# Optimization experiments

Measured on AMD Instinct MI355X. Metric: run time of the kernel, lower is better.

## Reference

```python
import jax, jax.numpy as jnp
import numpy as np

N_NODES, N_GRAPHS, PER_GRAPH, N_EDGES = 20000, 200, 100, 320000
X_DIM, E_DIM, G_DIM = 32, 16, 32
NUM_EMB, HEADS, LAYERS = 64, 2, 3
EPS_GEN, EPS_LN = 1e-7, 1e-5


def _w(k, shape, scale=0.05):
    return (jax.random.normal(k, shape) * scale).astype(jnp.float32)


def _mlp3(x, W1, b1, W2, b2, W3, b3):
    h = jax.nn.leaky_relu(x @ W1 + b1)
    h = jax.nn.leaky_relu(h @ W2 + b2)
    return h @ W3 + b3


def _seg_sum(x, idx, n):
    return jax.ops.segment_sum(x, idx, num_segments=n)


def _seg_mean(x, idx, n):
    s = _seg_sum(x, idx, n)
    cnt = _seg_sum(jnp.ones((x.shape[0],), x.dtype), idx, n)
    return s / jnp.clip(cnt, 1.0, None)[:, None]


def _seg_softmax(logits, idx, n):
    # PyG softmax: subtract per-segment max, normalize with +1e-16
    m = jax.ops.segment_max(logits, idx, num_segments=n)
    m = jnp.where(jnp.isfinite(m), m, 0.0)
    e = jnp.exp(logits - m[idx])
    s = jax.ops.segment_sum(e, idx, num_segments=n)
    return e / (s[idx] + 1e-16)


def _graph_layernorm(x, batch, n_graphs):
    # PyG LayerNorm(mode='graph', affine=False): mean/var over all node-feature
    # entries of each graph.
    f = x.shape[-1]
    cnt = _seg_sum(jnp.ones((x.shape[0],), x.dtype), batch, n_graphs)
    norm = jnp.clip(cnt, 1.0, None) * f
    mean = _seg_sum(x.sum(-1), batch, n_graphs) / norm
    xc = x - mean[batch][:, None]
    var = _seg_sum((xc * xc).sum(-1), batch, n_graphs) / norm
    return xc / jnp.sqrt(var + EPS_LN)[batch][:, None]


def _forward(x, edge_attr, cond, edge_index, batch,
             x2h_W1, x2h_b1, x2h_W2, x2h_b2, x2h_W3, x2h_b3,
             e2h_W1, e2h_b1, e2h_W2, e2h_b2, e2h_W3, e2h_b3,
             c2h_W1, c2h_b1, c2h_W2, c2h_b2, c2h_W3, c2h_b3,
             gen_W, tr_Wq, tr_bq, tr_Wk, tr_bk, tr_Wv, tr_bv, tr_We, tr_Ws, tr_bs,
             lin_W, lin_b, ff_W1, ff_b1, ff_W2, ff_b2):
    N = x.shape[0]
    G = cond.shape[0]
    Naug = N + G
    o = _mlp3(x, x2h_W1, x2h_b1, x2h_W2, x2h_b2, x2h_W3, x2h_b3)
    e = _mlp3(edge_attr, e2h_W1, e2h_b1, e2h_W2, e2h_b2, e2h_W3, e2h_b3)
    c = _mlp3(cond, c2h_W1, c2h_b1, c2h_W2, c2h_b2, c2h_W3, c2h_b3)
    # virtual-node edges: node<->virtual node of its graph (virtual ids = N..N+G-1)
    u = jnp.arange(N, dtype=edge_index.dtype)
    v = batch.astype(edge_index.dtype) + N
    aug_ei = jnp.concatenate([edge_index, jnp.stack([u, v]), jnp.stack([v, u])], axis=1)
    e_p = jnp.zeros((2 * N, NUM_EMB), o.dtype).at[:, 0].set(1.0)
    aug_e = jnp.concatenate([e, e_p], axis=0)
    # add_self_loops(fill_value='mean'): self-loop attr = mean of incoming edge attrs
    loop_attr = _seg_mean(aug_e, aug_ei[1], Naug)
    loops = jnp.arange(Naug, dtype=edge_index.dtype)
    aug_ei = jnp.concatenate([aug_ei, jnp.stack([loops, loops])], axis=1)
    aug_e = jnp.concatenate([aug_e, loop_attr], axis=0)
    aug_batch = jnp.concatenate([batch, jnp.arange(G, dtype=batch.dtype)])
    o = jnp.concatenate([o, c], axis=0)  # [Naug, emb]
    src, dst = aug_ei[0], aug_ei[1]
    scale = 1.0 / float(np.sqrt(NUM_EMB))
    for i in range(LAYERS):
        # GENConv(aggr='add', norm=None, num_layers=1): sum(relu(x_j+e)+eps) + x, then Linear
        msg = jax.nn.relu(o[src] + aug_e) + EPS_GEN
        agg = (_seg_sum(msg, dst, Naug) + o) @ gen_W[i]
        # TransformerConv(2*emb -> emb, heads, edge_dim=emb, concat=True)
        xin = jnp.concatenate([o, agg], axis=1)  # [Naug, 2*emb]
        q = (xin @ tr_Wq[i] + tr_bq[i]).reshape(Naug, HEADS, NUM_EMB)
        k = (xin @ tr_Wk[i] + tr_bk[i]).reshape(Naug, HEADS, NUM_EMB)
        vv = (xin @ tr_Wv[i] + tr_bv[i]).reshape(Naug, HEADS, NUM_EMB)
        eh = (aug_e @ tr_We[i]).reshape(-1, HEADS, NUM_EMB)  # [E, H, C]
        kj = k[src] + eh
        alpha = _seg_softmax(jnp.einsum('ehc,ehc->eh', q[dst], kj) * scale, dst, Naug)
        tout = _seg_sum((vv[src] + eh) * alpha[..., None], dst, Naug)
        tout = tout.reshape(Naug, HEADS * NUM_EMB) + xin @ tr_Ws[i] + tr_bs[i]
        # residual + graph LayerNorm, then FFN + graph LayerNorm
        o = _graph_layernorm(o + tout @ lin_W[i] + lin_b[i], aug_batch, G)
        ff = jax.nn.leaky_relu(o @ ff_W1[i] + ff_b1[i]) @ ff_W2[i] + ff_b2[i]
        o = _graph_layernorm(o + ff, aug_batch, G)
    node_o, virt = o[:N], o[N:]
    glob = jnp.concatenate([_seg_mean(node_o, batch, G), virt, c], axis=1)
    o_final = jnp.concatenate([node_o, c[batch]], axis=1)
    return (o_final, glob)


def setup_inputs() -> dict:
    key = jax.random.key(0)
    ks = iter(jax.random.split(key, 64))
    inp = {}
    inp['x'] = jax.random.normal(next(ks), (N_NODES, X_DIM), dtype=jnp.float32)
    inp['edge_attr'] = jax.random.normal(next(ks), (N_EDGES, E_DIM), dtype=jnp.float32)
    inp['cond'] = jax.random.normal(next(ks), (N_GRAPHS, G_DIM), dtype=jnp.float32)
    src = jax.random.randint(next(ks), (N_EDGES,), 0, N_NODES)
    dst = (src // PER_GRAPH) * PER_GRAPH + jax.random.randint(next(ks), (N_EDGES,), 0, PER_GRAPH)
    inp['edge_index'] = jnp.stack([src, dst]).astype(jnp.int32)
    inp['batch'] = jnp.repeat(jnp.arange(N_GRAPHS, dtype=jnp.int32), PER_GRAPH)
    for p, nin in [('x2h', X_DIM), ('e2h', E_DIM), ('c2h', G_DIM)]:
        inp[p + '_W1'] = _w(next(ks), (nin, NUM_EMB)); inp[p + '_b1'] = _w(next(ks), (NUM_EMB,))
        inp[p + '_W2'] = _w(next(ks), (NUM_EMB, NUM_EMB)); inp[p + '_b2'] = _w(next(ks), (NUM_EMB,))
        inp[p + '_W3'] = _w(next(ks), (NUM_EMB, NUM_EMB)); inp[p + '_b3'] = _w(next(ks), (NUM_EMB,))
    HC = HEADS * NUM_EMB
    inp['gen_W'] = _w(next(ks), (LAYERS, NUM_EMB, NUM_EMB))
    inp['tr_Wq'] = _w(next(ks), (LAYERS, 2 * NUM_EMB, HC)); inp['tr_bq'] = _w(next(ks), (LAYERS, HC))
    inp['tr_Wk'] = _w(next(ks), (LAYERS, 2 * NUM_EMB, HC)); inp['tr_bk'] = _w(next(ks), (LAYERS, HC))
    inp['tr_Wv'] = _w(next(ks), (LAYERS, 2 * NUM_EMB, HC)); inp['tr_bv'] = _w(next(ks), (LAYERS, HC))
    inp['tr_We'] = _w(next(ks), (LAYERS, NUM_EMB, HC))
    inp['tr_Ws'] = _w(next(ks), (LAYERS, 2 * NUM_EMB, HC)); inp['tr_bs'] = _w(next(ks), (LAYERS, HC))
    inp['lin_W'] = _w(next(ks), (LAYERS, HC, NUM_EMB)); inp['lin_b'] = _w(next(ks), (LAYERS, NUM_EMB))
    inp['ff_W1'] = _w(next(ks), (LAYERS, NUM_EMB, 4 * NUM_EMB)); inp['ff_b1'] = _w(next(ks), (LAYERS, 4 * NUM_EMB))
    inp['ff_W2'] = _w(next(ks), (LAYERS, 4 * NUM_EMB, NUM_EMB)); inp['ff_b2'] = _w(next(ks), (LAYERS, NUM_EMB))
    return inp


def reference(x, edge_attr, cond, edge_index, batch,
              x2h_W1, x2h_b1, x2h_W2, x2h_b2, x2h_W3, x2h_b3,
              e2h_W1, e2h_b1, e2h_W2, e2h_b2, e2h_W3, e2h_b3,
              c2h_W1, c2h_b1, c2h_W2, c2h_b2, c2h_W3, c2h_b3,
              gen_W, tr_Wq, tr_bq, tr_Wk, tr_bk, tr_Wv, tr_bv, tr_We, tr_Ws, tr_bs,
              lin_W, lin_b, ff_W1, ff_b1, ff_W2, ff_b2):
    return _forward(x, edge_attr, cond, edge_index, batch,
                    x2h_W1, x2h_b1, x2h_W2, x2h_b2, x2h_W3, x2h_b3,
                    e2h_W1, e2h_b1, e2h_W2, e2h_b2, e2h_W3, e2h_b3,
                    c2h_W1, c2h_b1, c2h_W2, c2h_b2, c2h_W3, c2h_b3,
                    gen_W, tr_Wq, tr_bq, tr_Wk, tr_bk, tr_Wv, tr_bv, tr_We, tr_Ws, tr_bs,
                    lin_W, lin_b, ff_W1, ff_b1, ff_W2, ff_b2)
```

## Files before the change

### kernel.cpp

```cpp
#include <hip/hip_runtime.h>
#include <cstddef>

#define NN   20000
#define NG   200
#define NE   320000
#define NAUG 20200
#define NE2  360000
#define EAUG 380200
#define DD   64
#define HC   128
#define QS   640

typedef float  f32x4 __attribute__((ext_vector_type(4)));
typedef short  s16x8 __attribute__((ext_vector_type(8)));

static __device__ __forceinline__ unsigned short bf16r(float f){
  unsigned u = __float_as_uint(f);
  u += 0x7FFFu + ((u >> 16) & 1u);
  return (unsigned short)(u >> 16);
}
static __device__ __forceinline__ float4 b2f4(ushort4 u){
  return make_float4(__uint_as_float((unsigned)u.x << 16),
                     __uint_as_float((unsigned)u.y << 16),
                     __uint_as_float((unsigned)u.z << 16),
                     __uint_as_float((unsigned)u.w << 16));
}
static __device__ __forceinline__ ushort4 f2b4(float4 v){
  ushort4 s; s.x=bf16r(v.x); s.y=bf16r(v.y); s.z=bf16r(v.z); s.w=bf16r(v.w); return s;
}
static __device__ __forceinline__ float d4(float4 a, float4 b){
  return a.x*b.x + a.y*b.y + a.z*b.z + a.w*b.w;
}
static __device__ __forceinline__ float4 f4a(float4 a, float4 b, float t){
  return make_float4(a.x + b.x*t, a.y + b.y*t, a.z + b.z*t, a.w + b.w*t);
}
static __device__ __forceinline__ float4 f4s(float4 a, float s){
  return make_float4(a.x*s, a.y*s, a.z*s, a.w*s);
}

#define WTAB_INIT { \
  {0,0,128,128,136,128,0},{0,0,128,128,136,128,16384},{0,0,128,128,136,128,32768}, \
  {1,0,128,128,136,128,0},{1,0,128,128,136,128,16384},{1,0,128,128,136,128,32768}, \
  {2,0,128,128,136,128,0},{2,0,128,128,136,128,16384},{2,0,128,128,136,128,32768}, \
  {3,0,128,128,136,128,0},{3,0,128,128,136,128,16384},{3,0,128,128,136,128,32768}, \
  {4,0,64,64,72,64,0},{4,0,64,64,72,64,4096},{4,0,64,64,72,64,8192}, \
  {5,0,128,64,136,64,0},{5,0,128,64,136,64,8192},{5,0,128,64,136,64,16384}, \
  {6,0,64,256,72,256,0},{6,0,64,256,72,256,16384},{6,0,64,256,72,256,32768}, \
  {7,0,256,64,264,64,0},{7,0,256,64,264,64,16384},{7,0,256,64,264,64,32768}, \
  {8,0,64,64,72,128,0},{8,0,64,64,72,128,64},{8,0,64,64,72,128,8192},{8,0,64,64,72,128,8256},{8,0,64,64,72,128,16384},{8,0,64,64,72,128,16448}, \
  {9,0,32,64,40,64,0},{10,0,64,64,72,64,0},{11,0,64,64,72,64,0}, \
  {12,0,16,64,40,64,0},{13,0,64,64,72,64,0},{14,0,64,64,72,64,0}, \
  {15,0,32,64,40,64,0},{16,0,64,64,72,64,0},{17,0,64,64,72,64,0} }

static const int WTAB_H[39][7] = WTAB_INIT;
__device__ static const int WTAB_D[39][7] = WTAB_INIT;

struct WPtrs { const float* p[18]; };

__global__ void wconv_all_k(WPtrs wp, unsigned short* __restrict__ outbase){
  int b = blockIdx.x;
  int acc = 0; unsigned ooff = 0;
  #pragma unroll 1
  for (int j = 0; j < 39; j++){
    int e  = WTAB_D[j][3] * WTAB_D[j][4];
    int nb = (e + 255) >> 8;
    if (b < acc + nb){
      int idx = (b - acc)*256 + threadIdx.x;
      if (idx < e){
        int KP = WTAB_D[j][4];
        int n = idx / KP, k = idx % KP;
        float v = 0.f;
        if (k < WTAB_D[j][2]){
          const float* s = wp.p[WTAB_D[j][0]];
          int st = WTAB_D[j][5], so = WTAB_D[j][6];
          v = (WTAB_D[j][1] == 0) ? s[(size_t)so + (size_t)k*st + n]
                                  : s[(size_t)so + (size_t)n*st + k];
        }
        outbase[ooff + idx] = bf16r(v);
      }
      return;
    }
    acc += nb; ooff += (unsigned)e;
  }
}

__global__ void qecomb_k(const float* __restrict__ trWq, const float* __restrict__ trbq,
                         const float* __restrict__ trWe,
                         unsigned short* __restrict__ qweb, float* __restrict__ bqeb){
  int L = blockIdx.y;
  int n = blockIdx.x;
  int i = threadIdx.x;
  int h = n >> 6, d = n & 63;
  const float* Wq = trWq + (size_t)L*128*128;
  const float* We = trWe + (size_t)L*64*128;
  float acc = 0.f;
  for (int c = 0; c < 64; c++)
    acc += Wq[(size_t)i*128 + h*64 + c] * We[(size_t)d*128 + h*64 + c];
  qweb[(size_t)L*128*136 + n*136 + i] = bf16r(acc);
  if (i < 8) qweb[(size_t)L*128*136 + n*136 + 128 + i] = 0;
  if (i == 0){
    const float* bq = trbq + (size_t)L*128;
    float b = 0.f;
    for (int c = 0; c < 64; c++) b += bq[h*64 + c] * We[(size_t)d*128 + h*64 + c];
    bqeb[L*128 + n] = b;
  }
}

template<int NT>
__launch_bounds__(256)
__global__ void gemm_mfma_k(const float* __restrict__ A, const float* __restrict__ A2,
                            int M, int K, int lda,
                            const unsigned short* __restrict__ WtG,
                            const float* __restrict__ bias, int act,
                            const float* __restrict__ res, const float* __restrict__ res2,
                            int rstride, float* __restrict__ out, int ostride){
  extern __shared__ unsigned short smem[];
  const int KC  = (K > 128) ? 128 : K;
  const int KPc = KC + 8;
  const int KP  = K + 8;
  unsigned short* Wts  = smem;
  unsigned short* Asub = smem + NT*KPc;
  const int tid = threadIdx.x;
  const int wid = tid >> 6, lane = tid & 63;
  const int lrow = lane & 15, quad = lane >> 4;
  const int m0 = blockIdx.x * 64;
  f32x4 acc[NT/16];
  #pragma unroll
  for (int t = 0; t < NT/16; t++) acc[t] = (f32x4){0.f,0.f,0.f,0.f};

  for (int k0 = 0; k0 < K; k0 += KC){
    const int wv = NT*KPc/8, wrow = KPc/8;
    for (int i = tid; i < wv; i += 256){
      int n = i / wrow, c8 = i % wrow;
      *(uint4*)&Wts[n*KPc + c8*8] = *(const uint4*)&WtG[(size_t)n*KP + k0 + c8*8];
    }
    const int av = 64*KC/4, arow = KC/4;
    for (int i = tid; i < av; i += 256){
      int r = i / arow, c4i = i % arow;
      int m = m0 + r, k = k0 + c4i*4;
      float4 v = make_float4(0.f,0.f,0.f,0.f);
      if (m < M){
        v = *(const float4*)(A + (size_t)m*lda + k);
        if (A2){ float4 w = *(const float4*)(A2 + (size_t)m*lda + k);
                 v.x += w.x; v.y += w.y; v.z += w.z; v.w += w.w; }
      }
      *(ushort4*)&Asub[r*KPc + c4i*4] = f2b4(v);
    }
    __syncthreads();
    const int ksteps = KC >> 5;
    for (int ks = 0; ks < ksteps; ks++){
      s16x8 a = *(const s16x8*)&Asub[(wid*16 + lrow)*KPc + ks*32 + quad*8];
      #pragma unroll
      for (int nt = 0; nt < NT/16; nt++){
        s16x8 b = *(const s16x8*)&Wts[(nt*16 + lrow)*KPc + ks*32 + quad*8];
        acc[nt] = __builtin_amdgcn_mfma_f32_16x16x32_bf16(a, b, acc[nt], 0, 0, 0);
      }
    }
    __syncthreads();
  }

  const int mb = m0 + wid*16 + quad*4;
  #pragma unroll
  for (int nt = 0; nt < NT/16; nt++){
    int n = nt*16 + lrow;
    #pragma unroll
    for (int r = 0; r < 4; r++){
      int m = mb + r;
      if (m < M){
        float v = acc[nt][r];
        if (bias) v += bias[n];
        if (act)  v = v > 0.f ? v : 0.01f*v;
        if (res)  v += res [(size_t)m*rstride + n];
        if (res2) v += res2[(size_t)m*rstride + n];
        out[(size_t)m*ostride + n] = v;
      }
    }
  }
}

struct PW5 { const unsigned short* w[5]; const float* b[5]; };

__launch_bounds__(256)
__global__ void qkvs5_k(const float* __restrict__ A, int M, PW5 pw,
                        float* __restrict__ out){
  __shared__ __align__(16) unsigned short Wts[128*136];
  __shared__ __align__(16) unsigned short Asub[64*136];
  const unsigned short* WtG = pw.w[blockIdx.y];
  const float* bias = pw.b[blockIdx.y];
  const int tid = threadIdx.x;
  const int wid = tid >> 6, lane = tid & 63;
  const int lrow = lane & 15, quad = lane >> 4;
  const int m0 = blockIdx.x * 64;
  for (int i = tid; i < 128*17; i += 256){
    int n = i/17, c8 = i%17;
    *(uint4*)&Wts[n*136 + c8*8] = *(const uint4*)&WtG[(size_t)n*136 + c8*8];
  }
  for (int i = tid; i < 64*32; i += 256){
    int r = i >> 5, c4 = (i & 31)*4;
    int m = m0 + r;
    float4 v = make_float4(0.f,0.f,0.f,0.f);
    if (m < M) v = *(const float4*)(A + (size_t)m*128 + c4);
    *(ushort4*)&Asub[r*136 + c4] = f2b4(v);
  }
  __syncthreads();
  f32x4 acc[8];
  #pragma unroll
  for (int t=0;t<8;t++) acc[t] = (f32x4){0.f,0.f,0.f,0.f};
  #pragma unroll
  for (int ks = 0; ks < 4; ks++){
    s16x8 a = *(const s16x8*)&Asub[(wid*16 + lrow)*136 + ks*32 + quad*8];
    #pragma unroll
    for (int nt = 0; nt < 8; nt++){
      s16x8 b = *(const s16x8*)&Wts[(nt*16 + lrow)*136 + ks*32 + quad*8];
      acc[nt] = __builtin_amdgcn_mfma_f32_16x16x32_bf16(a, b, acc[nt], 0, 0, 0);
    }
  }
  const int mb = m0 + wid*16 + quad*4;
  const int yoff = blockIdx.y*128;
  #pragma unroll
  for (int nt = 0; nt < 8; nt++){
    int n = nt*16 + lrow;
    #pragma unroll
    for (int r = 0; r < 4; r++){
      int m = mb + r;
      if (m < M) out[(size_t)m*QS + yoff + n] = acc[nt][r] + bias[n];
    }
  }
}

struct PW2 { const unsigned short* w[2]; };

__launch_bounds__(256)
__global__ void tout2_k(const float* __restrict__ wv, int M, PW2 pw,
                        const float* __restrict__ t1, const float* __restrict__ qkvs,
                        float* __restrict__ tout){
  __shared__ __align__(16) unsigned short Wts[64*72];
  __shared__ __align__(16) unsigned short Asub[64*72];
  const unsigned short* WtG = pw.w[blockIdx.y];
  const int tid = threadIdx.x;
  const int wid = tid >> 6, lane = tid & 63;
  const int lrow = lane & 15, quad = lane >> 4;
  const int m0 = blockIdx.x * 64;
  const int yoff = blockIdx.y * 64;
  for (int i = tid; i < 64*9; i += 256){
    int n = i/9, c8 = i%9;
    *(uint4*)&Wts[n*72 + c8*8] = *(const uint4*)&WtG[(size_t)n*72 + c8*8];
  }
  for (int i = tid; i < 64*16; i += 256){
    int r = i >> 4, c4 = (i & 15)*4;
    int m = m0 + r;
    float4 v = make_float4(0.f,0.f,0.f,0.f);
    if (m < M) v = *(const float4*)(wv + (size_t)m*HC + yoff + c4);
    *(ushort4*)&Asub[r*72 + c4] = f2b4(v);
  }
  __syncthreads();
  f32x4 acc[4];
  #pragma unroll
  for (int t=0;t<4;t++) acc[t] = (f32x4){0.f,0.f,0.f,0.f};
  #pragma unroll
  for (int ks = 0; ks < 2; ks++){
    s16x8 a = *(const s16x8*)&Asub[(wid*16 + lrow)*72 + ks*32 + quad*8];
    #pragma unroll
    for (int nt = 0; nt < 4; nt++){
      s16x8 b = *(const s16x8*)&Wts[(nt*16 + lrow)*72 + ks*32 + quad*8];
      acc[nt] = __builtin_amdgcn_mfma_f32_16x16x32_bf16(a, b, acc[nt], 0, 0, 0);
    }
  }
  const int mb = m0 + wid*16 + quad*4;
  #pragma unroll
  for (int nt = 0; nt < 4; nt++){
    int n = nt*16 + lrow;
    #pragma unroll
    for (int r = 0; r < 4; r++){
      int m = mb + r;
      if (m < M)
        tout[(size_t)m*HC + yoff + n] = acc[nt][r]
          + t1[(size_t)m*HC + yoff + n] + qkvs[(size_t)m*QS + 384 + yoff + n];
    }
  }
}

__launch_bounds__(256)
__global__ void mlp3_mfma_k(const float* __restrict__ X, int M, int Din,
                            const unsigned short* __restrict__ w1t,
                            const unsigned short* __restrict__ w2t,
                            const unsigned short* __restrict__ w3t,
                            const float* __restrict__ b1, const float* __restrict__ b2,
                            const float* __restrict__ b3,
                            const int* __restrict__ perm, float* __restrict__ out,
                            unsigned short* __restrict__ outb){
  __shared__ __align__(16) unsigned short W1s[64*40], W2s[64*72], W3s[64*72];
  __shared__ __align__(16) unsigned short xs[64*40], hs[64*72];
  __shared__ float bsh[192];
  const int tid = threadIdx.x;
  for (int i = tid; i < 320; i += 256)  *(uint4*)&W1s[i*8] = *(const uint4*)&w1t[i*8];
  for (int i = tid; i < 576; i += 256){ *(uint4*)&W2s[i*8] = *(const uint4*)&w2t[i*8];
                                        *(uint4*)&W3s[i*8] = *(const uint4*)&w3t[i*8]; }
  if (tid < 64){ bsh[tid] = b1[tid]; bsh[64+tid] = b2[tid]; bsh[128+tid] = b3[tid]; }
  const int m0 = blockIdx.x * 64;
  for (int i = tid; i < 512; i += 256){
    int r = i >> 3, c4 = (i & 7) * 4;
    int m = m0 + r;
    float4 v = make_float4(0.f,0.f,0.f,0.f);
    if (m < M && c4 < Din) v = *(const float4*)(X + (size_t)m*Din + c4);
    *(ushort4*)&xs[r*40 + c4] = f2b4(v);
  }
  __syncthreads();
  const int wid = tid >> 6, lane = tid & 63;
  const int lrow = lane & 15, quad = lane >> 4;
  f32x4 acc[4];

  #pragma unroll
  for (int t = 0; t < 4; t++) acc[t] = (f32x4){0.f,0.f,0.f,0.f};
  {
    s16x8 a = *(const s16x8*)&xs[(wid*16 + lrow)*40 + quad*8];
    #pragma unroll
    for (int nt = 0; nt < 4; nt++){
      s16x8 b = *(const s16x8*)&W1s[(nt*16 + lrow)*40 + quad*8];
      acc[nt] = __builtin_amdgcn_mfma_f32_16x16x32_bf16(a, b, acc[nt], 0, 0, 0);
    }
  }
  #pragma unroll
  for (int nt = 0; nt < 4; nt++){
    int n = nt*16 + lrow;
    #pragma unroll
    for (int r = 0; r < 4; r++){
      float v = acc[nt][r] + bsh[n];
      v = v > 0.f ? v : 0.01f*v;
      hs[(wid*16 + quad*4 + r)*72 + n] = bf16r(v);
    }
  }
  __syncthreads();

  #pragma unroll
  for (int t = 0; t < 4; t++) acc[t] = (f32x4){0.f,0.f,0.f,0.f};
  #pragma unroll
  for (int ks = 0; ks < 2; ks++){
    s16x8 a = *(const s16x8*)&hs[(wid*16 + lrow)*72 + ks*32 + quad*8];
    #pragma unroll
    for (int nt = 0; nt < 4; nt++){
      s16x8 b = *(const s16x8*)&W2s[(nt*16 + lrow)*72 + ks*32 + quad*8];
      acc[nt] = __builtin_amdgcn_mfma_f32_16x16x32_bf16(a, b, acc[nt], 0, 0, 0);
    }
  }
  __syncthreads();
  #pragma unroll
  for (int nt = 0; nt < 4; nt++){
    int n = nt*16 + lrow;
    #pragma unroll
    for (int r = 0; r < 4; r++){
      float v = acc[nt][r] + bsh[64 + n];
      v = v > 0.f ? v : 0.01f*v;
      hs[(wid*16 + quad*4 + r)*72 + n] = bf16r(v);
    }
  }
  __syncthreads();

  #pragma unroll
  for (int t = 0; t < 4; t++) acc[t] = (f32x4){0.f,0.f,0.f,0.f};
  #pragma unroll
  for (int ks = 0; ks < 2; ks++){
    s16x8 a = *(const s16x8*)&hs[(wid*16 + lrow)*72 + ks*32 + quad*8];
    #pragma unroll
    for (int nt = 0; nt < 4; nt++){
      s16x8 b = *(const s16x8*)&W3s[(nt*16 + lrow)*72 + ks*32 + quad*8];
      acc[nt] = __builtin_amdgcn_mfma_f32_16x16x32_bf16(a, b, acc[nt], 0, 0, 0);
    }
  }
  #pragma unroll
  for (int nt = 0; nt < 4; nt++){
    int n = nt*16 + lrow;
    #pragma unroll
    for (int r = 0; r < 4; r++){
      int m = m0 + wid*16 + quad*4 + r;
      if (m < M){
        int orow = perm ? perm[m] : m;
        float v = acc[nt][r] + bsh[128 + n];
        if (outb) outb[(size_t)orow*64 + n] = bf16r(v);
        else      out [(size_t)orow*64 + n] = v;
      }
    }
  }
}

__global__ void build_edges_k(const int* __restrict__ ei, const int* __restrict__ batch,
                              int* __restrict__ srcA, int* __restrict__ dstA){
  int idx = blockIdx.x*256 + threadIdx.x;
  if (idx >= EAUG) return;
  int s, d;
  if (idx < NE)          { s = ei[idx];              d = ei[NE+idx]; }
  else if (idx < NE+NN)  { int i = idx-NE;           s = i;            d = batch[i]+NN; }
  else if (idx < NE2)    { int i = idx-(NE+NN);      s = batch[i]+NN;  d = i; }
  else                   { int i = idx-NE2;          s = i;            d = i; }
  srcA[idx]=s; dstA[idx]=d;
}

__global__ void count_k(const int* __restrict__ dstA, int* __restrict__ cnt){
  int e = blockIdx.x*256 + threadIdx.x;
  if (e < EAUG) atomicAdd(&cnt[dstA[e]], 1);
}

__global__ void scan_k(const int* __restrict__ cnt, int* __restrict__ rowptr){
  __shared__ int part[1024];
  int tid = threadIdx.x;
  const int per = (NAUG + 1023) / 1024;
  int base = tid * per;
  int s = 0;
  for (int i=0;i<per;i++){ int idx=base+i; if (idx<NAUG) s += cnt[idx]; }
  part[tid] = s;
  __syncthreads();
  for (int off=1; off<1024; off<<=1){
    int v = (tid>=off) ? part[tid-off] : 0;
    __syncthreads();
    part[tid] += v;
    __syncthreads();
  }
  int run = (tid==0) ? 0 : part[tid-1];
  for (int i=0;i<per;i++){
    int idx=base+i;
    if (idx<NAUG){ rowptr[idx]=run; run += cnt[idx]; }
  }
  if (tid==0) rowptr[NAUG] = EAUG;
}

__global__ void scatter_k(const int* __restrict__ srcA, const int* __restrict__ dstA,
                          const int* __restrict__ rowptr, int* __restrict__ cursor,
                          int* __restrict__ esrc, int* __restrict__ epos,
                          int* __restrict__ pdst){
  int e = blockIdx.x*256 + threadIdx.x;
  if (e >= EAUG) return;
  int d = dstA[e];
  int pos = rowptr[d] + atomicAdd(&cursor[d], 1);
  esrc[pos] = srcA[e];
  pdst[pos] = d;
  epos[e]   = pos;
}

__global__ void set_ep_k(const int* __restrict__ epos, unsigned short* __restrict__ aug_b){
  int idx = blockIdx.x*256 + threadIdx.x;
  if (idx >= 2*NN*DD) return;
  int i = idx >> 6, c = idx & 63;
  aug_b[(size_t)epos[NE + i]*DD + c] = (c==0) ? (unsigned short)0x3F80 : (unsigned short)0;
}

__launch_bounds__(256)
__global__ void loopmean_k(const int* __restrict__ rowptr, const int* __restrict__ epos,
                           unsigned short* __restrict__ aug_b){
  int tid = threadIdx.x;
  int d = blockIdx.x*16 + (tid>>4);
  if (d >= NAUG) return;
  int t4 = (tid & 15)*4;
  int beg = rowptr[d], end = rowptr[d+1];
  int sp = epos[NE2 + d];
  float4 s = make_float4(0.f,0.f,0.f,0.f);
  for (int p=beg; p<end; p++){
    float4 a = b2f4(*(const ushort4*)(aug_b + (size_t)p*DD + t4));
    float w = (p == sp) ? 0.f : 1.f;
    s.x += w*a.x; s.y += w*a.y; s.z += w*a.z; s.w += w*a.w;
  }
  int n = end - beg - 1;
  float cv = (n < 1) ? 1.f : (float)n;
  *(ushort4*)(aug_b + (size_t)sp*DD + t4) = f2b4(f4s(s, 1.f/cv));
}

__launch_bounds__(512)
__global__ void msg_graph_k(const float* __restrict__ o, const unsigned short* __restrict__ aug_b,
                            const int* __restrict__ rowptr,
                            const int* __restrict__ esrc, float* __restrict__ aggsum){
  __shared__ __align__(16) float OS[101*72];
  __shared__ unsigned char EL[3072];
  const int g = blockIdx.x >> 1, half = blockIdx.x & 1;
  const int tid = threadIdx.x;
  for (int i = tid; i < 101*16; i += 512){
    int ln = i >> 4, c4 = (i & 15)*4;
    int row = (ln < 100) ? g*100 + ln : NN + g;
    *(float4*)&OS[ln*72 + c4] = *(const float4*)(o + (size_t)row*DD + c4);
  }
  const int baseA = rowptr[g*100];
  const int lenA  = rowptr[g*100 + 100] - baseA;
  const int baseB = rowptr[NN + g];
  const int lenB  = rowptr[NN + g + 1] - baseB;
  const bool useL = (lenA + lenB) <= 3072;
  if (useL){
    for (int i = tid; i < lenA; i += 512){
      int s = esrc[baseA + i];
      EL[i] = (unsigned char)((s >= NN) ? 100 : (s - g*100));
    }
    for (int i = tid; i < lenB; i += 512){
      int s = esrc[baseB + i];
      EL[lenA + i] = (unsigned char)((s >= NN) ? 100 : (s - g*100));
    }
  }
  __syncthreads();
  const int gr = tid >> 4, t4 = (tid & 15)*4;
  const int ld0 = half ? 51 : 0, ld1 = half ? 101 : 51;
  for (int ld = ld0 + gr; ld < ld1; ld += 32){
    int d, pbeg, pend, eofs;
    if (ld < 100){ d = g*100 + ld; pbeg = rowptr[d]; pend = rowptr[d+1]; eofs = -baseA; }
    else         { d = NN + g;     pbeg = baseB;     pend = baseB + lenB; eofs = lenA - baseB; }
    float4 acc = make_float4(0.f,0.f,0.f,0.f);
    for (int p = pbeg; p < pend; p++){
      int ls;
      if (useL) ls = EL[p + eofs];
      else { int s = esrc[p]; ls = (s >= NN) ? 100 : (s - g*100); }
      float4 ov = *(const float4*)&OS[ls*72 + t4];
      float4 ae = b2f4(*(const ushort4*)(aug_b + (size_t)p*DD + t4));
      acc.x += fmaxf(ov.x+ae.x, 0.f) + 1e-7f;
      acc.y += fmaxf(ov.y+ae.y, 0.f) + 1e-7f;
      acc.z += fmaxf(ov.z+ae.z, 0.f) + 1e-7f;
      acc.w += fmaxf(ov.w+ae.w, 0.f) + 1e-7f;
    }
    *(float4*)(aggsum + (size_t)d*DD + t4) = acc;
  }
}

__global__ void copy_o_xin_k(const float* __restrict__ o, float* __restrict__ xin){
  int idx = blockIdx.x*256 + threadIdx.x;
  if (idx >= NAUG*DD) return;
  int n = idx >> 6, c = idx & 63;
  xin[(size_t)n*HC + c] = o[idx];
}

__launch_bounds__(512)
__global__ void scoredot_k(const float* __restrict__ qkvs,
                           const unsigned short* __restrict__ aug_b,
                           const int* __restrict__ pdst, const int* __restrict__ esrc,
                           float2* __restrict__ lg){
  int p = blockIdx.x*32 + (threadIdx.x >> 4);
  if (p >= EAUG) return;
  int t4 = (threadIdx.x & 15)*4;
  int d = pdst[p], s = esrc[p];
  const float* qr = qkvs + (size_t)d*QS;
  const float* kr = qkvs + (size_t)s*QS + 128;
  float4 q0  = *(const float4*)(qr + t4);
  float4 q1  = *(const float4*)(qr + 64 + t4);
  float4 qe0 = *(const float4*)(qr + 512 + t4);
  float4 qe1 = *(const float4*)(qr + 576 + t4);
  float4 k0  = *(const float4*)(kr + t4);
  float4 k1  = *(const float4*)(kr + 64 + t4);
  float4 ae  = b2f4(*(const ushort4*)(aug_b + (size_t)p*DD + t4));
  float p0 = d4(q0,k0) + d4(qe0,ae);
  float p1 = d4(q1,k1) + d4(qe1,ae);
  p0 += __shfl_xor(p0,8); p0 += __shfl_xor(p0,4); p0 += __shfl_xor(p0,2); p0 += __shfl_xor(p0,1);
  p1 += __shfl_xor(p1,8); p1 += __shfl_xor(p1,4); p1 += __shfl_xor(p1,2); p1 += __shfl_xor(p1,1);
  if ((threadIdx.x & 15) == 0) lg[p] = make_float2(p0*0.125f, p1*0.125f);
}

__launch_bounds__(512)
__global__ void attn_lite_k(const float* __restrict__ qkvs, const float2* __restrict__ lg,
                            const int* __restrict__ rowptr, const int* __restrict__ esrc,
                            float* __restrict__ t1, float2* __restrict__ m2,
                            float2* __restrict__ linv2){
  __shared__ __align__(16) unsigned short VS[101*128];
  __shared__ unsigned char EL[3072];
  const int g = blockIdx.x >> 1, half = blockIdx.x & 1;
  const int tid = threadIdx.x;
  for (int i = tid; i < 101*32; i += 512){
    int ln = i >> 5, c4 = (i & 31)*4;
    int row = (ln < 100) ? g*100 + ln : NN + g;
    float4 v = *(const float4*)(qkvs + (size_t)row*QS + 256 + c4);
    *(ushort4*)&VS[ln*128 + c4] = f2b4(v);
  }
  const int baseA = rowptr[g*100];
  const int lenA  = rowptr[g*100 + 100] - baseA;
  const int baseB = rowptr[NN + g];
  const int lenB  = rowptr[NN + g + 1] - baseB;
  const bool useL = (lenA + lenB) <= 3072;
  if (useL){
    for (int i = tid; i < lenA; i += 512){
      int s = esrc[baseA + i];
      EL[i] = (unsigned char)((s >= NN) ? 100 : (s - g*100));
    }
    for (int i = tid; i < lenB; i += 512){
      int s = esrc[baseB + i];
      EL[lenA + i] = (unsigned char)((s >= NN) ? 100 : (s - g*100));
    }
  }
  __syncthreads();
  const int gr = tid >> 4, t4 = (tid & 15)*4;
  const int ld0 = half ? 51 : 0, ld1 = half ? 101 : 51;
  for (int ld = ld0 + gr; ld < ld1; ld += 32){
    int d, pbeg, pend, eofs;
    if (ld < 100){ d = g*100 + ld; pbeg = rowptr[d]; pend = rowptr[d+1]; eofs = -baseA; }
    else         { d = NN + g;     pbeg = baseB;     pend = baseB + lenB; eofs = lenA - baseB; }
    float m0 = -1e30f, m1 = -1e30f;
    for (int p = pbeg; p < pend; p++){
      float2 lv = lg[p];
      m0 = fmaxf(m0, lv.x); m1 = fmaxf(m1, lv.y);
    }
    float l0 = 0.f, l1 = 0.f;
    float4 a0 = make_float4(0.f,0.f,0.f,0.f), a1 = a0;
    for (int p = pbeg; p < pend; p++){
      float2 lv = lg[p];
      int ls;
      if (useL) ls = EL[p + eofs];
      else { int s = esrc[p]; ls = (s >= NN) ? 100 : (s - g*100); }
      const unsigned short* vr = &VS[ls*128];
      float4 v0 = b2f4(*(const ushort4*)(vr + t4));
      float4 v1 = b2f4(*(const ushort4*)(vr + 64 + t4));
      float e0 = __expf(lv.x - m0);
      float e1 = __expf(lv.y - m1);
      l0 += e0; a0 = f4a(a0, v0, e0);
      l1 += e1; a1 = f4a(a1, v1, e1);
    }
    float i0 = 1.f/(l0 + 1e-16f), i1 = 1.f/(l1 + 1e-16f);
    *(float4*)(t1 + (size_t)d*HC + t4)      = f4s(a0, i0);
    *(float4*)(t1 + (size_t)d*HC + 64 + t4) = f4s(a1, i1);
    if ((tid & 15) == 0){
      m2[d]    = make_float2(m0, m1);
      linv2[d] = make_float2(i0, i1);
    }
  }
}

__launch_bounds__(256)
__global__ void wsum_k(const unsigned short* __restrict__ aug_b, const float2* __restrict__ lg,
                       const float2* __restrict__ m2, const float2* __restrict__ linv2,
                       const int* __restrict__ rowptr, float* __restrict__ wbuf){
  int tid = threadIdx.x;
  int d = blockIdx.x*16 + (tid>>4);
  if (d >= NAUG) return;
  int t4 = (tid & 15)*4;
  float2 m = m2[d];
  float2 li = linv2[d];
  float4 w0 = make_float4(0.f,0.f,0.f,0.f), w1 = w0;
  int beg = rowptr[d], end = rowptr[d+1];
  for (int p = beg; p < end; p++){
    float2 lv = lg[p];
    float4 ae = b2f4(*(const ushort4*)(aug_b + (size_t)p*DD + t4));
    float a0 = __expf(lv.x - m.x) * li.x;
    float a1 = __expf(lv.y - m.y) * li.y;
    w0 = f4a(w0, ae, a0);
    w1 = f4a(w1, ae, a1);
  }
  *(float4*)(wbuf + (size_t)d*HC + t4)      = w0;
  *(float4*)(wbuf + (size_t)d*HC + 64 + t4) = w1;
}

__global__ void ln_k(const float* __restrict__ y, float* __restrict__ o,
                     float* __restrict__ xin){
  int g = blockIdx.x, tid = threadIdx.x;
  float sum=0.f, ss=0.f;
  for (int i=tid; i<101*64; i+=256){
    int nd=i>>6, c=i&63;
    int row = (nd<100) ? g*100+nd : NN+g;
    float v = y[(size_t)row*DD + c];
    sum += v; ss += v*v;
  }
  #pragma unroll
  for (int off=32; off; off>>=1){ sum += __shfl_xor(sum, off); ss += __shfl_xor(ss, off); }
  __shared__ float s1[4], s2[4];
  if ((tid&63)==0){ s1[tid>>6]=sum; s2[tid>>6]=ss; }
  __syncthreads();
  sum = s1[0]+s1[1]+s1[2]+s1[3];
  ss  = s2[0]+s2[1]+s2[2]+s2[3];
  const float inv = 1.f/6464.f;
  float mean = sum*inv;
  float var  = ss*inv - mean*mean;
  float rstd = rsqrtf(var + 1e-5f);
  for (int i=tid; i<101*64; i+=256){
    int nd=i>>6, c=i&63;
    int row = (nd<100) ? g*100+nd : NN+g;
    float v = (y[(size_t)row*DD + c] - mean)*rstd;
    o[(size_t)row*DD + c] = v;
    if (xin) xin[(size_t)row*HC + c] = v;
  }
}

__global__ void copy_c_o_k(const float* __restrict__ c_emb, float* __restrict__ o){
  int idx = blockIdx.x*256 + threadIdx.x;
  if (idx >= NG*DD) return;
  o[(size_t)NN*DD + idx] = c_emb[idx];
}

__global__ void glob_k(const float* __restrict__ o, const float* __restrict__ c_emb,
                       float* __restrict__ gout){
  int g = blockIdx.x, c = threadIdx.x;
  float acc = 0.f;
  for (int t=0;t<100;t++) acc += o[(size_t)(g*100+t)*DD + c];
  gout[(size_t)g*192 + c]       = acc / 100.f;
  gout[(size_t)g*192 + 64 + c]  = o[(size_t)(NN+g)*DD + c];
  gout[(size_t)g*192 + 128 + c] = c_emb[(size_t)g*DD + c];
}
__global__ void ofinal_k(const float* __restrict__ o, const float* __restrict__ c_emb,
                         const int* __restrict__ batch, float* __restrict__ out){
  int idx = blockIdx.x*256 + threadIdx.x;
  if (idx >= NN*HC) return;
  int n = idx>>7, j = idx&127;
  out[idx] = (j<64) ? o[(size_t)n*DD + j] : c_emb[(size_t)batch[n]*DD + (j-64)];
}

static inline int cdiv(int a, int b){ return (a+b-1)/b; }

static inline void gemm_mfma(int N, const float* A, const float* A2, int M, int K, int lda,
                             const unsigned short* Wt, const float* bias, int act,
                             const float* res, const float* res2, int rstride,
                             float* out, int ostride, hipStream_t st){
  int KC = (K > 128) ? 128 : K;
  int KPc = KC + 8;
  size_t sh = (size_t)(N*KPc + 64*KPc) * 2;
  int grid = cdiv(M, 64);
  if (N == 64)
    gemm_mfma_k<64><<<grid,256,sh,st>>>(A,A2,M,K,lda,Wt,bias,act,res,res2,rstride,out,ostride);
  else if (N == 128)
    gemm_mfma_k<128><<<grid,256,sh,st>>>(A,A2,M,K,lda,Wt,bias,act,res,res2,rstride,out,ostride);
  else
    gemm_mfma_k<256><<<grid,256,sh,st>>>(A,A2,M,K,lda,Wt,bias,act,res,res2,rstride,out,ostride);
}

extern "C" void kernel_launch(void* const* d_in, const int* in_sizes, int n_in,
                              void* d_out, int out_size, void* d_ws, size_t ws_size,
                              hipStream_t stream){
  (void)in_sizes; (void)n_in; (void)out_size;
  const float* x         = (const float*)d_in[0];
  const float* edge_attr = (const float*)d_in[1];
  const float* cond      = (const float*)d_in[2];
  const int*   edge_index= (const int*)  d_in[3];
  const int*   batch     = (const int*)  d_in[4];
  const float* xW1=(const float*)d_in[5],  *xb1=(const float*)d_in[6],
             * xW2=(const float*)d_in[7],  *xb2=(const float*)d_in[8],
             * xW3=(const float*)d_in[9],  *xb3=(const float*)d_in[10];
  const float* eW1=(const float*)d_in[11], *eb1=(const float*)d_in[12],
             * eW2=(const float*)d_in[13], *eb2=(const float*)d_in[14],
             * eW3=(const float*)d_in[15], *eb3=(const float*)d_in[16];
  const float* cW1=(const float*)d_in[17], *cb1=(const float*)d_in[18],
             * cW2=(const float*)d_in[19], *cb2=(const float*)d_in[20],
             * cW3=(const float*)d_in[21], *cb3=(const float*)d_in[22];
  const float* gen_W=(const float*)d_in[23];
  const float* trWq=(const float*)d_in[24], *trbq=(const float*)d_in[25];
  const float* trWk=(const float*)d_in[26], *trbk=(const float*)d_in[27];
  const float* trWv=(const float*)d_in[28], *trbv=(const float*)d_in[29];
  const float* trWe=(const float*)d_in[30];
  const float* trWs=(const float*)d_in[31], *trbs=(const float*)d_in[32];
  const float* linW=(const float*)d_in[33], *linb=(const float*)d_in[34];
  const float* ffW1=(const float*)d_in[35], *ffb1=(const float*)d_in[36];
  const float* ffW2=(const float*)d_in[37], *ffb2=(const float*)d_in[38];
  float* out = (float*)d_out;

  float* ws = (float*)d_ws;
  size_t off = 0;
  auto alloc = [&](size_t n)->float*{ float* p = ws + off; off += (n + 63) & ~(size_t)63; return p; };
  int*      srcA  = (int*)alloc(EAUG);
  int*      dstA  = (int*)alloc(EAUG);
  int*      cnt   = (int*)alloc(NAUG);
  int*      rowptr= (int*)alloc(NAUG+1);
  int*      cursor= (int*)alloc(NAUG);
  int*      esrc  = (int*)alloc(EAUG);
  int*      epos  = (int*)alloc(EAUG);
  int*      pdst  = (int*)alloc(EAUG);
  unsigned short* aug_b = (unsigned short*)alloc((size_t)EAUG*DD/2);
  float*    o     = alloc((size_t)NAUG*DD);
  float*    c_emb = alloc((size_t)NG*DD);
  float*    ybuf  = alloc((size_t)NAUG*DD);
  float*    aggsum= alloc((size_t)NAUG*DD);
  float*    xin   = alloc((size_t)NAUG*HC);
  float*    xqkvs = alloc((size_t)NAUG*QS);
  float*    toutb = alloc((size_t)NAUG*HC);
  float*    t1    = alloc((size_t)NAUG*HC);
  float*    wbuf  = alloc((size_t)NAUG*HC);
  float*    ffh   = alloc((size_t)NAUG*256);
  float2*   lgb   = (float2*)alloc((size_t)EAUG*2);
  float2*   m2v   = (float2*)alloc((size_t)NAUG*2);
  float2*   li2v  = (float2*)alloc((size_t)NAUG*2);
  unsigned short* warena = (unsigned short*)alloc(210432);
  unsigned short* qweb   = (unsigned short*)alloc(3*128*136/2 + 64);
  float*    bqeb  = alloc(3*128);
  if (off*sizeof(float) > ws_size) return;

  const unsigned short* wptr[39];
  int wblk = 0;
  { size_t woff = 0;
    for (int j = 0; j < 39; j++){
      wptr[j] = warena + woff;
      int e = WTAB_H[j][3]*WTAB_H[j][4];
      woff += (size_t)e;
      wblk += cdiv(e, 256);
    } }

  WPtrs wp;
  wp.p[0]=trWq; wp.p[1]=trWk; wp.p[2]=trWv; wp.p[3]=trWs; wp.p[4]=gen_W;
  wp.p[5]=linW; wp.p[6]=ffW1; wp.p[7]=ffW2; wp.p[8]=trWe;
  wp.p[9]=xW1; wp.p[10]=xW2; wp.p[11]=xW3;
  wp.p[12]=eW1; wp.p[13]=eW2; wp.p[14]=eW3;
  wp.p[15]=cW1; wp.p[16]=cW2; wp.p[17]=cW3;
  wconv_all_k<<<wblk,256,0,stream>>>(wp, warena);
  qecomb_k<<<dim3(128,3),128,0,stream>>>(trWq, trbq, trWe, qweb, bqeb);

  build_edges_k<<<cdiv(EAUG,256),256,0,stream>>>(edge_index, batch, srcA, dstA);
  hipMemsetAsync(cnt, 0, sizeof(int)*NAUG, stream);
  hipMemsetAsync(cursor, 0, sizeof(int)*NAUG, stream);
  count_k<<<cdiv(EAUG,256),256,0,stream>>>(dstA, cnt);
  scan_k<<<1,1024,0,stream>>>(cnt, rowptr);
  scatter_k<<<cdiv(EAUG,256),256,0,stream>>>(srcA, dstA, rowptr, cursor, esrc, epos, pdst);

  mlp3_mfma_k<<<cdiv(NN,64),256,0,stream>>>(x,        NN, 32, wptr[30],wptr[31],wptr[32], xb1,xb2,xb3, nullptr, o,     nullptr);
  mlp3_mfma_k<<<cdiv(NG,64),256,0,stream>>>(cond,     NG, 32, wptr[36],wptr[37],wptr[38], cb1,cb2,cb3, nullptr, c_emb, nullptr);
  mlp3_mfma_k<<<cdiv(NE,64),256,0,stream>>>(edge_attr,NE, 16, wptr[33],wptr[34],wptr[35], eb1,eb2,eb3, epos,    nullptr, aug_b);
  set_ep_k<<<cdiv(2*NN*DD,256),256,0,stream>>>(epos, aug_b);
  loopmean_k<<<cdiv(NAUG,16),256,0,stream>>>(rowptr, epos, aug_b);
  copy_c_o_k<<<cdiv(NG*DD,256),256,0,stream>>>(c_emb, o);
  copy_o_xin_k<<<cdiv(NAUG*DD,256),256,0,stream>>>(o, xin);

  for (int L=0; L<3; L++){
    const float* lb_i = linb + (size_t)L*DD;
    const float* f1b  = ffb1 + (size_t)L*256;
    const float* f2b  = ffb2 + (size_t)L*DD;
    const unsigned short* genT = wptr[12+L], *linT = wptr[15+L], *ff1T = wptr[18+L], *ff2T = wptr[21+L];
    PW5 pw5;
    pw5.w[0]=wptr[0+L]; pw5.w[1]=wptr[3+L]; pw5.w[2]=wptr[6+L]; pw5.w[3]=wptr[9+L];
    pw5.w[4]=qweb + (size_t)L*128*136;
    pw5.b[0]=trbq+(size_t)L*HC; pw5.b[1]=trbk+(size_t)L*HC;
    pw5.b[2]=trbv+(size_t)L*HC; pw5.b[3]=trbs+(size_t)L*HC;
    pw5.b[4]=bqeb + (size_t)L*128;
    PW2 pwT; pwT.w[0]=wptr[24+2*L]; pwT.w[1]=wptr[25+2*L];

    msg_graph_k<<<2*NG,512,0,stream>>>(o, aug_b, rowptr, esrc, aggsum);
    gemm_mfma( 64, aggsum, o, NAUG, 64, 64, genT, nullptr, 0, nullptr, nullptr, 0, xin+64, HC, stream);
    qkvs5_k<<<dim3(cdiv(NAUG,64),5),256,0,stream>>>(xin, NAUG, pw5, xqkvs);
    scoredot_k<<<cdiv(EAUG,32),512,0,stream>>>(xqkvs, aug_b, pdst, esrc, lgb);
    attn_lite_k<<<2*NG,512,0,stream>>>(xqkvs, lgb, rowptr, esrc, t1, m2v, li2v);
    wsum_k<<<cdiv(NAUG,16),256,0,stream>>>(aug_b, lgb, m2v, li2v, rowptr, wbuf);
    tout2_k<<<dim3(cdiv(NAUG,64),2),256,0,stream>>>(wbuf, NAUG, pwT, t1, xqkvs, toutb);
    gemm_mfma( 64, toutb, nullptr, NAUG, 128, 128, linT, lb_i, 0, o, nullptr, DD, ybuf, DD, stream);
    ln_k<<<NG,256,0,stream>>>(ybuf, o, nullptr);
    gemm_mfma(256, o,   nullptr, NAUG,  64,  64, ff1T, f1b, 1, nullptr, nullptr, 0, ffh, 256, stream);
    gemm_mfma( 64, ffh, nullptr, NAUG, 256, 256, ff2T, f2b, 0, o, nullptr, DD, ybuf, DD, stream);
    ln_k<<<NG,256,0,stream>>>(ybuf, o, xin);
  }

  glob_k<<<NG,64,0,stream>>>(o, c_emb, out + (size_t)NN*HC);
  ofinal_k<<<cdiv(NN*HC,256),256,0,stream>>>(o, c_emb, batch, out);
}
```

Before: 1.316 ms.

## Fuse edge-weighted sum into attention kernel and restructure CSR build

New measurement: 1.283 ms. 1.03x faster.

```diff
diff --git a/kernel.cpp b/kernel.cpp
--- a/kernel.cpp
+++ b/kernel.cpp
@@ -290,30 +290,36 @@
                             const int* __restrict__ perm, float* __restrict__ out,
                             unsigned short* __restrict__ outb){
   __shared__ __align__(16) unsigned short W1s[64*40], W2s[64*72], W3s[64*72];
-  __shared__ __align__(16) unsigned short xs[64*40], hs[64*72];
+  __shared__ __align__(16) unsigned short xs[4][16*40];
+  __shared__ __align__(16) unsigned short hs[4][16*72];
   __shared__ float bsh[192];
   const int tid = threadIdx.x;
+  const int wid = tid >> 6, lane = tid & 63;
+  const int lrow = lane & 15, quad = lane >> 4;
   for (int i = tid; i < 320; i += 256)  *(uint4*)&W1s[i*8] = *(const uint4*)&w1t[i*8];
   for (int i = tid; i < 576; i += 256){ *(uint4*)&W2s[i*8] = *(const uint4*)&w2t[i*8];
                                         *(uint4*)&W3s[i*8] = *(const uint4*)&w3t[i*8]; }
   if (tid < 64){ bsh[tid] = b1[tid]; bsh[64+tid] = b2[tid]; bsh[128+tid] = b3[tid]; }
-  const int m0 = blockIdx.x * 64;
-  for (int i = tid; i < 512; i += 256){
-    int r = i >> 3, c4 = (i & 7) * 4;
+
+  const int m0 = blockIdx.x*64 + wid*16;
+  {
+    int r = lane >> 2, c8 = (lane & 3) * 8;
     int m = m0 + r;
-    float4 v = make_float4(0.f,0.f,0.f,0.f);
-    if (m < M && c4 < Din) v = *(const float4*)(X + (size_t)m*Din + c4);
-    *(ushort4*)&xs[r*40 + c4] = f2b4(v);
+    float4 va = make_float4(0.f,0.f,0.f,0.f), vb = va;
+    if (m < M && c8 < Din){
+      va = *(const float4*)(X + (size_t)m*Din + c8);
+      vb = *(const float4*)(X + (size_t)m*Din + c8 + 4);
+    }
+    *(ushort4*)&xs[wid][r*40 + c8]     = f2b4(va);
+    *(ushort4*)&xs[wid][r*40 + c8 + 4] = f2b4(vb);
   }
   __syncthreads();
-  const int wid = tid >> 6, lane = tid & 63;
-  const int lrow = lane & 15, quad = lane >> 4;
+
   f32x4 acc[4];
-
   #pragma unroll
   for (int t = 0; t < 4; t++) acc[t] = (f32x4){0.f,0.f,0.f,0.f};
   {
-    s16x8 a = *(const s16x8*)&xs[(wid*16 + lrow)*40 + quad*8];
+    s16x8 a = *(const s16x8*)&xs[wid][lrow*40 + quad*8];
     #pragma unroll
     for (int nt = 0; nt < 4; nt++){
       s16x8 b = *(const s16x8*)&W1s[(nt*16 + lrow)*40 + quad*8];
@@ -327,23 +333,20 @@
     for (int r = 0; r < 4; r++){
       float v = acc[nt][r] + bsh[n];
       v = v > 0.f ? v : 0.01f*v;
-      hs[(wid*16 + quad*4 + r)*72 + n] = bf16r(v);
-    }
-  }
-  __syncthreads();
-
+      hs[wid][(quad*4 + r)*72 + n] = bf16r(v);
+    }
+  }
   #pragma unroll
   for (int t = 0; t < 4; t++) acc[t] = (f32x4){0.f,0.f,0.f,0.f};
   #pragma unroll
   for (int ks = 0; ks < 2; ks++){
-    s16x8 a = *(const s16x8*)&hs[(wid*16 + lrow)*72 + ks*32 + quad*8];
+    s16x8 a = *(const s16x8*)&hs[wid][lrow*72 + ks*32 + quad*8];
     #pragma unroll
     for (int nt = 0; nt < 4; nt++){
       s16x8 b = *(const s16x8*)&W2s[(nt*16 + lrow)*72 + ks*32 + quad*8];
       acc[nt] = __builtin_amdgcn_mfma_f32_16x16x32_bf16(a, b, acc[nt], 0, 0, 0);
     }
   }
-  __syncthreads();
   #pragma unroll
   for (int nt = 0; nt < 4; nt++){
     int n = nt*16 + lrow;
@@ -351,16 +354,14 @@
     for (int r = 0; r < 4; r++){
       float v = acc[nt][r] + bsh[64 + n];
       v = v > 0.f ? v : 0.01f*v;
-      hs[(wid*16 + quad*4 + r)*72 + n] = bf16r(v);
-    }
-  }
-  __syncthreads();
-
+      hs[wid][(quad*4 + r)*72 + n] = bf16r(v);
+    }
+  }
   #pragma unroll
   for (int t = 0; t < 4; t++) acc[t] = (f32x4){0.f,0.f,0.f,0.f};
   #pragma unroll
   for (int ks = 0; ks < 2; ks++){
-    s16x8 a = *(const s16x8*)&hs[(wid*16 + lrow)*72 + ks*32 + quad*8];
+    s16x8 a = *(const s16x8*)&hs[wid][lrow*72 + ks*32 + quad*8];
     #pragma unroll
     for (int nt = 0; nt < 4; nt++){
       s16x8 b = *(const s16x8*)&W3s[(nt*16 + lrow)*72 + ks*32 + quad*8];
@@ -372,7 +373,7 @@
     int n = nt*16 + lrow;
     #pragma unroll
     for (int r = 0; r < 4; r++){
-      int m = m0 + wid*16 + quad*4 + r;
+      int m = m0 + quad*4 + r;
       if (m < M){
         int orow = perm ? perm[m] : m;
         float v = acc[nt][r] + bsh[128 + n];
@@ -384,7 +385,8 @@
 }
 
 __global__ void build_edges_k(const int* __restrict__ ei, const int* __restrict__ batch,
-                              int* __restrict__ srcA, int* __restrict__ dstA){
+                              int* __restrict__ srcA, int* __restrict__ dstA,
+                              int* __restrict__ cnt){
   int idx = blockIdx.x*256 + threadIdx.x;
   if (idx >= EAUG) return;
   int s, d;
@@ -393,11 +395,7 @@
   else if (idx < NE2)    { int i = idx-(NE+NN);      s = batch[i]+NN;  d = i; }
   else                   { int i = idx-NE2;          s = i;            d = i; }
   srcA[idx]=s; dstA[idx]=d;
-}
-
-__global__ void count_k(const int* __restrict__ dstA, int* __restrict__ cnt){
-  int e = blockIdx.x*256 + threadIdx.x;
-  if (e < EAUG) atomicAdd(&cnt[dstA[e]], 1);
+  atomicAdd(&cnt[d], 1);
 }
 
 __global__ void scan_k(const int* __restrict__ cnt, int* __restrict__ rowptr){
@@ -423,17 +421,30 @@
   if (tid==0) rowptr[NAUG] = EAUG;
 }
 
-__global__ void scatter_k(const int* __restrict__ srcA, const int* __restrict__ dstA,
+__global__ void scatter_k(const int* __restrict__ dstA,
                           const int* __restrict__ rowptr, int* __restrict__ cursor,
-                          int* __restrict__ esrc, int* __restrict__ epos,
-                          int* __restrict__ pdst){
+                          int* __restrict__ eid, int* __restrict__ epos){
   int e = blockIdx.x*256 + threadIdx.x;
   if (e >= EAUG) return;
   int d = dstA[e];
   int pos = rowptr[d] + atomicAdd(&cursor[d], 1);
-  esrc[pos] = srcA[e];
-  pdst[pos] = d;
-  epos[e]   = pos;
+  eid[pos] = e;
+  epos[e]  = pos;
+}
+
+__global__ void fill_esrc_k(const int* __restrict__ eid, const int* __restrict__ srcA,
+                            int* __restrict__ esrc){
+  int p = blockIdx.x*256 + threadIdx.x;
+  if (p < EAUG) esrc[p] = srcA[eid[p]];
+}
+
+__launch_bounds__(256)
+__global__ void fill_pdst_k(const int* __restrict__ rowptr, int* __restrict__ pdst){
+  int d = blockIdx.x*16 + (threadIdx.x >> 4);
+  if (d >= NAUG) return;
+  int lane = threadIdx.x & 15;
+  int beg = rowptr[d], end = rowptr[d+1];
+  for (int p = beg + lane; p < end; p += 16) pdst[p] = d;
 }
 
 __global__ void set_ep_k(const int* __restrict__ epos, unsigned short* __restrict__ aug_b){
@@ -548,9 +559,9 @@
 
 __launch_bounds__(512)
 __global__ void attn_lite_k(const float* __restrict__ qkvs, const float2* __restrict__ lg,
+                            const unsigned short* __restrict__ aug_b,
                             const int* __restrict__ rowptr, const int* __restrict__ esrc,
-                            float* __restrict__ t1, float2* __restrict__ m2,
-                            float2* __restrict__ linv2){
+                            float* __restrict__ t1, float* __restrict__ wbuf){
   __shared__ __align__(16) unsigned short VS[101*128];
   __shared__ unsigned char EL[3072];
   const int g = blockIdx.x >> 1, half = blockIdx.x & 1;
@@ -589,7 +600,7 @@
       m0 = fmaxf(m0, lv.x); m1 = fmaxf(m1, lv.y);
     }
     float l0 = 0.f, l1 = 0.f;
-    float4 a0 = make_float4(0.f,0.f,0.f,0.f), a1 = a0;
+    float4 a0 = make_float4(0.f,0.f,0.f,0.f), a1 = a0, w0 = a0, w1 = a0;
     for (int p = pbeg; p < pend; p++){
       float2 lv = lg[p];
       int ls;
@@ -598,43 +609,18 @@
       const unsigned short* vr = &VS[ls*128];
       float4 v0 = b2f4(*(const ushort4*)(vr + t4));
       float4 v1 = b2f4(*(const ushort4*)(vr + 64 + t4));
+      float4 ae = b2f4(*(const ushort4*)(aug_b + (size_t)p*DD + t4));
       float e0 = __expf(lv.x - m0);
       float e1 = __expf(lv.y - m1);
-      l0 += e0; a0 = f4a(a0, v0, e0);
-      l1 += e1; a1 = f4a(a1, v1, e1);
+      l0 += e0; a0 = f4a(a0, v0, e0); w0 = f4a(w0, ae, e0);
+      l1 += e1; a1 = f4a(a1, v1, e1); w1 = f4a(w1, ae, e1);
     }
     float i0 = 1.f/(l0 + 1e-16f), i1 = 1.f/(l1 + 1e-16f);
-    *(float4*)(t1 + (size_t)d*HC + t4)      = f4s(a0, i0);
-    *(float4*)(t1 + (size_t)d*HC + 64 + t4) = f4s(a1, i1);
-    if ((tid & 15) == 0){
-      m2[d]    = make_float2(m0, m1);
-      linv2[d] = make_float2(i0, i1);
-    }
-  }
-}
-
-__launch_bounds__(256)
-__global__ void wsum_k(const unsigned short* __restrict__ aug_b, const float2* __restrict__ lg,
-                       const float2* __restrict__ m2, const float2* __restrict__ linv2,
-                       const int* __restrict__ rowptr, float* __restrict__ wbuf){
-  int tid = threadIdx.x;
-  int d = blockIdx.x*16 + (tid>>4);
-  if (d >= NAUG) return;
-  int t4 = (tid & 15)*4;
-  float2 m = m2[d];
-  float2 li = linv2[d];
-  float4 w0 = make_float4(0.f,0.f,0.f,0.f), w1 = w0;
-  int beg = rowptr[d], end = rowptr[d+1];
-  for (int p = beg; p < end; p++){
-    float2 lv = lg[p];
-    float4 ae = b2f4(*(const ushort4*)(aug_b + (size_t)p*DD + t4));
-    float a0 = __expf(lv.x - m.x) * li.x;
-    float a1 = __expf(lv.y - m.y) * li.y;
-    w0 = f4a(w0, ae, a0);
-    w1 = f4a(w1, ae, a1);
-  }
-  *(float4*)(wbuf + (size_t)d*HC + t4)      = w0;
-  *(float4*)(wbuf + (size_t)d*HC + 64 + t4) = w1;
+    *(float4*)(t1   + (size_t)d*HC + t4)      = f4s(a0, i0);
+    *(float4*)(t1   + (size_t)d*HC + 64 + t4) = f4s(a1, i1);
+    *(float4*)(wbuf + (size_t)d*HC + t4)      = f4s(w0, i0);
+    *(float4*)(wbuf + (size_t)d*HC + 64 + t4) = f4s(w1, i1);
+  }
 }
 
 __global__ void ln_k(const float* __restrict__ y, float* __restrict__ o,
@@ -745,6 +731,7 @@
   int*      cnt   = (int*)alloc(NAUG);
   int*      rowptr= (int*)alloc(NAUG+1);
   int*      cursor= (int*)alloc(NAUG);
+  int*      eid   = (int*)alloc(EAUG);
   int*      esrc  = (int*)alloc(EAUG);
   int*      epos  = (int*)alloc(EAUG);
   int*      pdst  = (int*)alloc(EAUG);
@@ -760,8 +747,6 @@
   float*    wbuf  = alloc((size_t)NAUG*HC);
   float*    ffh   = alloc((size_t)NAUG*256);
   float2*   lgb   = (float2*)alloc((size_t)EAUG*2);
-  float2*   m2v   = (float2*)alloc((size_t)NAUG*2);
-  float2*   li2v  = (float2*)alloc((size_t)NAUG*2);
   unsigned short* warena = (unsigned short*)alloc(210432);
   unsigned short* qweb   = (unsigned short*)alloc(3*128*136/2 + 64);
   float*    bqeb  = alloc(3*128);
@@ -786,12 +771,13 @@
   wconv_all_k<<<wblk,256,0,stream>>>(wp, warena);
   qecomb_k<<<dim3(128,3),128,0,stream>>>(trWq, trbq, trWe, qweb, bqeb);
 
-  build_edges_k<<<cdiv(EAUG,256),256,0,stream>>>(edge_index, batch, srcA, dstA);
   hipMemsetAsync(cnt, 0, sizeof(int)*NAUG, stream);
   hipMemsetAsync(cursor, 0, sizeof(int)*NAUG, stream);
-  count_k<<<cdiv(EAUG,256),256,0,stream>>>(dstA, cnt);
+  build_edges_k<<<cdiv(EAUG,256),256,0,stream>>>(edge_index, batch, srcA, dstA, cnt);
   scan_k<<<1,1024,0,stream>>>(cnt, rowptr);
-  scatter_k<<<cdiv(EAUG,256),256,0,stream>>>(srcA, dstA, rowptr, cursor, esrc, epos, pdst);
+  scatter_k<<<cdiv(EAUG,256),256,0,stream>>>(dstA, rowptr, cursor, eid, epos);
+  fill_esrc_k<<<cdiv(EAUG,256),256,0,stream>>>(eid, srcA, esrc);
+  fill_pdst_k<<<cdiv(NAUG,16),256,0,stream>>>(rowptr, pdst);
 
   mlp3_mfma_k<<<cdiv(NN,64),256,0,stream>>>(x,        NN, 32, wptr[30],wptr[31],wptr[32], xb1,xb2,xb3, nullptr, o,     nullptr);
   mlp3_mfma_k<<<cdiv(NG,64),256,0,stream>>>(cond,     NG, 32, wptr[36],wptr[37],wptr[38], cb1,cb2,cb3, nullptr, c_emb, nullptr);
@@ -818,8 +804,7 @@
     gemm_mfma( 64, aggsum, o, NAUG, 64, 64, genT, nullptr, 0, nullptr, nullptr, 0, xin+64, HC, stream);
     qkvs5_k<<<dim3(cdiv(NAUG,64),5),256,0,stream>>>(xin, NAUG, pw5, xqkvs);
     scoredot_k<<<cdiv(EAUG,32),512,0,stream>>>(xqkvs, aug_b, pdst, esrc, lgb);
-    attn_lite_k<<<2*NG,512,0,stream>>>(xqkvs, lgb, rowptr, esrc, t1, m2v, li2v);
-    wsum_k<<<cdiv(NAUG,16),256,0,stream>>>(aug_b, lgb, m2v, li2v, rowptr, wbuf);
+    attn_lite_k<<<2*NG,512,0,stream>>>(xqkvs, lgb, aug_b, rowptr, esrc, t1, wbuf);
     tout2_k<<<dim3(cdiv(NAUG,64),2),256,0,stream>>>(wbuf, NAUG, pwT, t1, xqkvs, toutb);
     gemm_mfma( 64, toutb, nullptr, NAUG, 128, 128, linT, lb_i, 0, o, nullptr, DD, ybuf, DD, stream);
     ln_k<<<NG,256,0,stream>>>(ybuf, o, nullptr);
```
